# Performance work log

Hardware: AMD Instinct MI355X
Metric: run time of the kernel (lower is better)

## Reference

```python
import jax, jax.numpy as jnp
import numpy as np

ALPHA = 0.2  # LeakyReLU negative slope

def setup_inputs() -> dict:
    key = jax.random.key(0)
    k1, k2, k3 = jax.random.split(key, 3)
    B, N, F, H = 2, 4096, 512, 8
    d = F // H  # per-head in/out dim = 64
    h = jax.random.normal(k1, (B, N, F), dtype=jnp.float32)
    # xavier-uniform-like scale (gain 1.414, fan 64+64)
    W = jax.random.normal(k2, (H, d, d), dtype=jnp.float32) * 0.15
    a = jax.random.normal(k3, (H, 2 * d), dtype=jnp.float32) * 0.15
    return {"h": h, "W": W, "a": a}

def reference(h, W, a):
    B, N, F = h.shape
    H, _, o = W.shape
    d = F // H
    # split features per head: [B, H, N, d]
    hh = h.reshape(B, N, H, d).transpose(0, 2, 1, 3)
    Wh = jnp.einsum('bhnd,hdo->bhno', hh, W)          # [B,H,N,o]
    a1, a2 = a[:, :o], a[:, o:]
    Wh1 = jnp.einsum('bhno,ho->bhn', Wh, a1)          # [B,H,N]
    Wh2 = jnp.einsum('bhno,ho->bhn', Wh, a2)          # [B,H,N]
    e = jax.nn.leaky_relu(Wh1[..., :, None] + Wh2[..., None, :], ALPHA)  # [B,H,N,N]
    att = jax.nn.softmax(e, axis=-1)
    h_prime = jnp.einsum('bhnm,bhmo->bhno', att, Wh)  # [B,H,N,o]
    out = jax.nn.elu(h_prime)                         # concat=True -> ELU
    # concat heads along feature dim: [B, N, H*o]
    return out.transpose(0, 2, 1, 3).reshape(B, N, H * o)
```

## Files before the change

kernel.cpp:

```cpp
#include <hip/hip_runtime.h>
#include <hip/hip_fp16.h>


#define NB   2
#define NN   4096
#define NH   8
#define ALPHA 0.2f
#define LOG2E 1.4426950408889634f

typedef _Float16 f16x8 __attribute__((ext_vector_type(8)));
typedef _Float16 f16x2 __attribute__((ext_vector_type(2)));
typedef float    f32x4 __attribute__((ext_vector_type(4)));

__device__ __forceinline__ float dot2acc(f16x2 a, f16x2 b, float c) {
#if __has_builtin(__builtin_amdgcn_fdot2)
    return __builtin_amdgcn_fdot2(a, b, c, false);
#else
    return c + (float)a[0] * (float)b[0] + (float)a[1] * (float)b[1];
#endif
}

__global__ __launch_bounds__(256) void k_wh(
    const float* __restrict__ hsrc, const float* __restrict__ W,
    const float* __restrict__ a,
    _Float16* __restrict__ Wh_p, float* __restrict__ fb, float* __restrict__ gb)
{
    const int bid  = blockIdx.x;
    const int tile = bid & 63;
    const int bh   = bid >> 6;
    const int hh   = bh & 7;
    const int b    = bh >> 3;
    const int n0   = tile * 64;
    const int t    = threadIdx.x;
    const int w    = t >> 6;
    const int l    = t & 63;
    const int lr   = l & 15;
    const int lg   = l >> 4;

    __shared__ _Float16 __attribute__((aligned(16))) Wt16[64 * 88];
    __shared__ float red[2 * 64 * 16];

    {
        const float* Wg = W + hh * 4096;
        const int c  = t & 63;
        const int kq = (t >> 6) * 16;
        #pragma unroll
        for (int j = 0; j < 16; j++)
            Wt16[c * 88 + kq + j] = (_Float16)Wg[(kq + j) * 64 + c];
    }

    const float* hrow = hsrc + ((size_t)(b * NN + n0 + w * 16 + lr)) * 512
                        + hh * 64 + lg * 8;
    f16x8 afr[2];
    #pragma unroll
    for (int kh = 0; kh < 2; kh++) {
        float4 u0 = *(const float4*)(hrow + kh * 32);
        float4 u1 = *(const float4*)(hrow + kh * 32 + 4);
        f16x8 v;
        v[0] = (_Float16)u0.x; v[1] = (_Float16)u0.y;
        v[2] = (_Float16)u0.z; v[3] = (_Float16)u0.w;
        v[4] = (_Float16)u1.x; v[5] = (_Float16)u1.y;
        v[6] = (_Float16)u1.z; v[7] = (_Float16)u1.w;
        afr[kh] = v;
    }
    __syncthreads();

    f32x4 acc[4];
    #pragma unroll
    for (int ct = 0; ct < 4; ct++) acc[ct] = (f32x4){0.f, 0.f, 0.f, 0.f};
    #pragma unroll
    for (int kh = 0; kh < 2; kh++)
        #pragma unroll
        for (int ct = 0; ct < 4; ct++) {
            f16x8 bfr = *(const f16x8*)(&Wt16[(ct * 16 + lr) * 88 + kh * 32 + lg * 8]);
            acc[ct] = __builtin_amdgcn_mfma_f32_16x16x32_f16(afr[kh], bfr, acc[ct], 0, 0, 0);
        }

    {
        float a1v[4], a2v[4];
        const float* ag = a + hh * 128;
        #pragma unroll
        for (int ct = 0; ct < 4; ct++) {
            a1v[ct] = ag[ct * 16 + lr];
            a2v[ct] = ag[64 + ct * 16 + lr];
        }
        #pragma unroll
        for (int reg = 0; reg < 4; reg++) {
            float fp = 0.f, gp = 0.f;
            #pragma unroll
            for (int ct = 0; ct < 4; ct++) {
                fp = fmaf(acc[ct][reg], a1v[ct], fp);
                gp = fmaf(acc[ct][reg], a2v[ct], gp);
            }
            int row = w * 16 + lg * 4 + reg;
            red[0 * 1024 + row * 16 + lr] = fp;
            red[1 * 1024 + row * 16 + lr] = gp;
        }
    }
    __syncthreads();

    _Float16* wt = Wt16;
    #pragma unroll
    for (int ct = 0; ct < 4; ct++)
        #pragma unroll
        for (int reg = 0; reg < 4; reg++)
            wt[(ct * 16 + lr) * 88 + w * 16 + lg * 4 + reg] = (_Float16)acc[ct][reg];
    __syncthreads();

    if (t < 128) {
        int which = t >> 6, row = t & 63;
        const float* rr = &red[which * 1024 + row * 16];
        float s = 0.f;
        #pragma unroll
        for (int j = 0; j < 16; j++) s += rr[j];
        s *= LOG2E;
        float* dst = which ? gb : fb;
        dst[(size_t)bh * NN + n0 + row] = s;
    }

    #pragma unroll
    for (int p = 0; p < 2; p++) {
        int idx = t + p * 256;
        int ms  = idx >> 8;
        int ct  = (idx >> 6) & 3;
        int l2  = idx & 63;
        f16x8 v = *(const f16x8*)(&wt[(ct * 16 + (l2 & 15)) * 88 + ms * 32 + (l2 >> 4) * 8]);
        *(f16x8*)(Wh_p + (size_t)bh * 64 * NN
                       + (((size_t)(tile * 2 + ms) * 4 + ct) * 64 + l2) * 8) = v;
    }
}

__global__ __launch_bounds__(256) void k_prep(const float* __restrict__ gball,
                                              float* __restrict__ G,
                                              char* __restrict__ egfg_base)
{
    int bh = blockIdx.x, t = threadIdx.x;
    const float* g = gball + (size_t)bh * NN;
    float vals[16];
    float m = -1e30f;
    #pragma unroll
    for (int j = 0; j < 16; j++) { vals[j] = g[t + j * 256]; m = fmaxf(m, vals[j]); }
    #pragma unroll
    for (int s = 1; s < 64; s <<= 1) m = fmaxf(m, __shfl_xor(m, s, 64));
    __shared__ float wm[4];
    if ((t & 63) == 0) wm[t >> 6] = m;
    __syncthreads();
    float Gv = fmaxf(fmaxf(wm[0], wm[1]), fmaxf(wm[2], wm[3]));
    if (t == 0) G[bh] = Gv;
    _Float16* Eg = (_Float16*)(egfg_base + (size_t)bh * 16384);
    _Float16* Fg = Eg + NN;
    #pragma unroll
    for (int j = 0; j < 16; j++) {
        int i = t + j * 256;
        float d = vals[j] - Gv;
        Eg[i] = (_Float16)exp2f(d);
        Fg[i] = (_Float16)exp2f(ALPHA * d);
    }
}

__global__ __launch_bounds__(256, 3) void k_attn(
    const _Float16* __restrict__ Wh_p, const float* __restrict__ fb,
    const float* __restrict__ G, const char* __restrict__ egfg_base,
    float* __restrict__ out)
{
    const int orig  = blockIdx.x;
    const int bid   = (orig & 7) * 64 + (orig >> 3);
    const int ntile = bid & 31;
    const int bh    = bid >> 5;
    const int hh    = bh & 7;
    const int b     = bh >> 3;
    const int n0    = ntile * 128;
    const int t     = threadIdx.x;
    const int w     = t >> 6;
    const int l     = t & 63;
    const int kg    = w >> 1;
    const int wr    = w & 1;
    const int lr    = l & 15;
    const int lg    = l >> 4;

    const _Float16* Pp  = Wh_p + (size_t)bh * 64 * NN;
    const _Float16* Egp = (const _Float16*)(egfg_base + (size_t)bh * 16384);
    const float     Gv  = G[bh];

    f16x2 ef2[4], ff2[4];
    #pragma unroll
    for (int rg = 0; rg < 4; rg++) {
        int rn = n0 + wr * 64 + rg * 16 + lr;
        float s  = fb[(size_t)bh * NN + rn] + Gv;
        float t1 = (1.f - ALPHA) * s;
        _Float16 e = (_Float16)exp2f(fminf(t1, 0.f));
        _Float16 f = (_Float16)exp2f(fminf(-t1, 0.f));
        ef2[rg] = (f16x2){e, e};
        ff2[rg] = (f16x2){f, f};
    }
    const f16x2 one2 = (f16x2){(_Float16)1.0f, (_Float16)1.0f};

    f32x4 acc[4][4];
    #pragma unroll
    for (int rg = 0; rg < 4; rg++)
        #pragma unroll
        for (int ct = 0; ct < 4; ct++) acc[rg][ct] = (f32x4){0.f, 0.f, 0.f, 0.f};
    float dsum[4] = {0.f, 0.f, 0.f, 0.f};

    const _Float16* bp  = Pp + (size_t)kg * 64 * 2048 + (size_t)l * 8;
    const _Float16* ep  = Egp + kg * 2048 + lg * 8;
    const _Float16* epf = ep + NN;

    #define LOADSET(B0,B1,B2,B3,EG,FG)                                          \
        {                                                                        \
            B0 = *(const f16x8*)(bp);         B1 = *(const f16x8*)(bp + 512);    \
            B2 = *(const f16x8*)(bp + 1024);  B3 = *(const f16x8*)(bp + 1536);   \
            EG = *(const f16x8*)ep;           FG = *(const f16x8*)epf;           \
            bp += 2048; ep += 32; epf += 32;                                     \
        }

    #define COMPUTE(B0,B1,B2,B3,EG,FG)                                          \
        {                                                                        \
            _Pragma("unroll")                                                    \
            for (int rg = 0; rg < 4; rg++) {                                     \
                f16x8 af; float ds = dsum[rg];                                   \
                _Pragma("unroll")                                                \
                for (int d = 0; d < 4; d++) {                                    \
                    f16x2 e2 = ((const f16x2*)&(EG))[d];                         \
                    f16x2 f2 = ((const f16x2*)&(FG))[d];                         \
                    f16x2 p2 = __builtin_elementwise_max(e2 * ef2[rg],           \
                                                         f2 * ff2[rg]);          \
                    ((f16x2*)&af)[d] = p2;                                       \
                    ds = dot2acc(p2, one2, ds);                                  \
                }                                                                \
                dsum[rg] = ds;                                                   \
                acc[rg][0] = __builtin_amdgcn_mfma_f32_16x16x32_f16(             \
                    af, B0, acc[rg][0], 0, 0, 0);                                \
                acc[rg][1] = __builtin_amdgcn_mfma_f32_16x16x32_f16(             \
                    af, B1, acc[rg][1], 0, 0, 0);                                \
                acc[rg][2] = __builtin_amdgcn_mfma_f32_16x16x32_f16(             \
                    af, B2, acc[rg][2], 0, 0, 0);                                \
                acc[rg][3] = __builtin_amdgcn_mfma_f32_16x16x32_f16(             \
                    af, B3, acc[rg][3], 0, 0, 0);                                \
            }                                                                    \
        }

    f16x8 a0, a1, a2, a3, ae, az;
    f16x8 c0, c1, c2, c3, ce, cz;
    LOADSET(a0, a1, a2, a3, ae, az);

    #pragma clang loop unroll(disable)
    for (int hs = 0; hs < 64; hs += 2) {
        LOADSET(c0, c1, c2, c3, ce, cz);
        COMPUTE(a0, a1, a2, a3, ae, az);
        if (hs + 2 < 64) LOADSET(a0, a1, a2, a3, ae, az);
        COMPUTE(c0, c1, c2, c3, ce, cz);
    }
    #undef LOADSET
    #undef COMPUTE

    __shared__ f32x4 __attribute__((aligned(16))) Rw[2][16 * 64];
    __shared__ float dnP[256];
    __shared__ float dnS[128];

    #pragma unroll
    for (int rg = 0; rg < 4; rg++) {
        float d = dsum[rg];
        d += __shfl_xor(d, 16, 64);
        d += __shfl_xor(d, 32, 64);
        if (lg == 0) dnP[kg * 128 + wr * 64 + rg * 16 + lr] = d;
    }

    if (kg == 1) {
        #pragma unroll
        for (int rg = 0; rg < 4; rg++)
            #pragma unroll
            for (int ct = 0; ct < 4; ct++)
                Rw[wr][(rg * 4 + ct) * 64 + l] = acc[rg][ct];
    }
    __syncthreads();

    if (kg == 0) {
        dnS[wr * 64 + l] = dnP[wr * 64 + l] + dnP[128 + wr * 64 + l];
        float* outp = out + ((size_t)(b * NN + n0)) * 512 + hh * 64;
        #pragma unroll
        for (int rg = 0; rg < 4; rg++)
            #pragma unroll
            for (int reg = 0; reg < 4; reg++) {
                int row = wr * 64 + rg * 16 + lg * 4 + reg;
                float rinv = 1.0f / dnS[row];
                #pragma unroll
                for (int ct = 0; ct < 4; ct++) {
                    float v = (acc[rg][ct][reg] + Rw[wr][(rg * 4 + ct) * 64 + l][reg])
                              * rinv;
                    v = v > 0.f ? v : (exp2f(v * LOG2E) - 1.f);
                    outp[(size_t)row * 512 + ct * 16 + lr] = v;
                }
            }
    }
}

extern "C" void kernel_launch(void* const* d_in, const int* in_sizes, int n_in,
                              void* d_out, int out_size, void* d_ws, size_t ws_size,
                              hipStream_t stream)
{
    const float* hsrc = (const float*)d_in[0];
    const float* W    = (const float*)d_in[1];
    const float* a    = (const float*)d_in[2];
    float* outp       = (float*)d_out;

    const size_t WHT_BYTES = (size_t)NB * NH * 64 * NN * sizeof(_Float16);
    const size_t FB_BYTES  = (size_t)NB * NH * NN * sizeof(float);
    const size_t GB_BYTES  = (size_t)NB * NH * NN * sizeof(float);
    const size_t NEED = WHT_BYTES + FB_BYTES + GB_BYTES + 64 * sizeof(float);
    if (ws_size < NEED) return;

    char* ws = (char*)d_ws;
    _Float16* Wh_p = (_Float16*)ws;
    float*    fbuf = (float*)(ws + WHT_BYTES);
    char*     gbase = ws + WHT_BYTES + FB_BYTES;
    float*    Gmax = (float*)(ws + WHT_BYTES + FB_BYTES + GB_BYTES);

    k_wh  <<<dim3(NB * NH * (NN / 64)),  dim3(256), 0, stream>>>(hsrc, W, a, Wh_p, fbuf, (float*)gbase);
    k_prep<<<dim3(NB * NH),              dim3(256), 0, stream>>>((const float*)gbase, Gmax, gbase);
    k_attn<<<dim3(NB * NH * (NN / 128)), dim3(256), 0, stream>>>(Wh_p, fbuf, Gmax, gbase, outp);
}
```

Measured before the change: 57.15 us.

## Enlarge attention tile to 256 rows with 512 threads and four K-split groups

The attention kernel now computes 256 output rows per block using 8 waves. Each wave covers 128 rows, so every loaded Wh/Eg/Fg fragment feeds twice as many MFMAs, and the key dimension is split across four groups instead of two. The aim is to halve global B-operand traffic per output row. In exchange, accumulator registers double, which risks spills under the 512x2 launch bound. The grid halves, lowering occupancy, and the cross-group reduction through LDS becomes serialized over several barriers.

```diff
diff --git a/kernel.cpp b/kernel.cpp
--- a/kernel.cpp
+++ b/kernel.cpp
@@ -158,18 +158,18 @@
     }
 }
 
-__global__ __launch_bounds__(256, 3) void k_attn(
+__global__ __launch_bounds__(512, 2) void k_attn(
     const _Float16* __restrict__ Wh_p, const float* __restrict__ fb,
     const float* __restrict__ G, const char* __restrict__ egfg_base,
     float* __restrict__ out)
 {
     const int orig  = blockIdx.x;
-    const int bid   = (orig & 7) * 64 + (orig >> 3);
-    const int ntile = bid & 31;
-    const int bh    = bid >> 5;
+    const int bid   = (orig & 7) * 32 + (orig >> 3);
+    const int ntile = bid & 15;
+    const int bh    = bid >> 4;
     const int hh    = bh & 7;
     const int b     = bh >> 3;
-    const int n0    = ntile * 128;
+    const int n0    = ntile * 256;
     const int t     = threadIdx.x;
     const int w     = t >> 6;
     const int l     = t & 63;
@@ -182,10 +182,10 @@
     const _Float16* Egp = (const _Float16*)(egfg_base + (size_t)bh * 16384);
     const float     Gv  = G[bh];
 
-    f16x2 ef2[4], ff2[4];
-    #pragma unroll
-    for (int rg = 0; rg < 4; rg++) {
-        int rn = n0 + wr * 64 + rg * 16 + lr;
+    f16x2 ef2[8], ff2[8];
+    #pragma unroll
+    for (int rg = 0; rg < 8; rg++) {
+        int rn = n0 + wr * 128 + rg * 16 + lr;
         float s  = fb[(size_t)bh * NN + rn] + Gv;
         float t1 = (1.f - ALPHA) * s;
         _Float16 e = (_Float16)exp2f(fminf(t1, 0.f));
@@ -195,15 +195,15 @@
     }
     const f16x2 one2 = (f16x2){(_Float16)1.0f, (_Float16)1.0f};
 
-    f32x4 acc[4][4];
-    #pragma unroll
-    for (int rg = 0; rg < 4; rg++)
+    f32x4 acc[8][4];
+    #pragma unroll
+    for (int rg = 0; rg < 8; rg++)
         #pragma unroll
         for (int ct = 0; ct < 4; ct++) acc[rg][ct] = (f32x4){0.f, 0.f, 0.f, 0.f};
-    float dsum[4] = {0.f, 0.f, 0.f, 0.f};
-
-    const _Float16* bp  = Pp + (size_t)kg * 64 * 2048 + (size_t)l * 8;
-    const _Float16* ep  = Egp + kg * 2048 + lg * 8;
+    float dsum[8] = {0.f, 0.f, 0.f, 0.f, 0.f, 0.f, 0.f, 0.f};
+
+    const _Float16* bp  = Pp + (size_t)kg * 32 * 2048 + (size_t)l * 8;
+    const _Float16* ep  = Egp + kg * 1024 + lg * 8;
     const _Float16* epf = ep + NN;
 
     #define LOADSET(B0,B1,B2,B3,EG,FG)                                          \
@@ -217,7 +217,7 @@
     #define COMPUTE(B0,B1,B2,B3,EG,FG)                                          \
         {                                                                        \
             _Pragma("unroll")                                                    \
-            for (int rg = 0; rg < 4; rg++) {                                     \
+            for (int rg = 0; rg < 8; rg++) {                                     \
                 f16x8 af; float ds = dsum[rg];                                   \
                 _Pragma("unroll")                                                \
                 for (int d = 0; d < 4; d++) {                                    \
@@ -245,54 +245,67 @@
     LOADSET(a0, a1, a2, a3, ae, az);
 
     #pragma clang loop unroll(disable)
-    for (int hs = 0; hs < 64; hs += 2) {
+    for (int hs = 0; hs < 32; hs += 2) {
         LOADSET(c0, c1, c2, c3, ce, cz);
         COMPUTE(a0, a1, a2, a3, ae, az);
-        if (hs + 2 < 64) LOADSET(a0, a1, a2, a3, ae, az);
+        if (hs + 2 < 32) LOADSET(a0, a1, a2, a3, ae, az);
         COMPUTE(c0, c1, c2, c3, ce, cz);
     }
     #undef LOADSET
     #undef COMPUTE
 
-    __shared__ f32x4 __attribute__((aligned(16))) Rw[2][16 * 64];
-    __shared__ float dnP[256];
-    __shared__ float dnS[128];
-
-    #pragma unroll
-    for (int rg = 0; rg < 4; rg++) {
+    __shared__ f32x4 __attribute__((aligned(16))) Rw[2][32 * 64];
+    __shared__ float dnP[1024];
+    __shared__ float dnS[256];
+
+    #pragma unroll
+    for (int rg = 0; rg < 8; rg++) {
         float d = dsum[rg];
         d += __shfl_xor(d, 16, 64);
         d += __shfl_xor(d, 32, 64);
-        if (lg == 0) dnP[kg * 128 + wr * 64 + rg * 16 + lr] = d;
-    }
-
-    if (kg == 1) {
-        #pragma unroll
-        for (int rg = 0; rg < 4; rg++)
-            #pragma unroll
-            for (int ct = 0; ct < 4; ct++)
-                Rw[wr][(rg * 4 + ct) * 64 + l] = acc[rg][ct];
-    }
+        if (lg == 0) dnP[kg * 256 + wr * 128 + rg * 16 + lr] = d;
+    }
+
+    #define WRITE_R()                                                            \
+        { _Pragma("unroll") for (int rg = 0; rg < 8; rg++)                       \
+          _Pragma("unroll") for (int ct = 0; ct < 4; ct++)                       \
+            Rw[wr][(rg * 4 + ct) * 64 + l] = acc[rg][ct]; }
+    #define ADD_R()                                                              \
+        { _Pragma("unroll") for (int rg = 0; rg < 8; rg++)                       \
+          _Pragma("unroll") for (int ct = 0; ct < 4; ct++)                       \
+            acc[rg][ct] += Rw[wr][(rg * 4 + ct) * 64 + l]; }
+
+    if (kg == 1) WRITE_R();
+    __syncthreads();
+    if (t < 256) dnS[t] = dnP[t] + dnP[256 + t] + dnP[512 + t] + dnP[768 + t];
+    if (kg == 0) ADD_R();
+    __syncthreads();
+    if (kg == 2) WRITE_R();
+    __syncthreads();
+    if (kg == 0) ADD_R();
+    __syncthreads();
+    if (kg == 3) WRITE_R();
     __syncthreads();
 
     if (kg == 0) {
-        dnS[wr * 64 + l] = dnP[wr * 64 + l] + dnP[128 + wr * 64 + l];
+        ADD_R();
         float* outp = out + ((size_t)(b * NN + n0)) * 512 + hh * 64;
         #pragma unroll
-        for (int rg = 0; rg < 4; rg++)
+        for (int rg = 0; rg < 8; rg++)
             #pragma unroll
             for (int reg = 0; reg < 4; reg++) {
-                int row = wr * 64 + rg * 16 + lg * 4 + reg;
+                int row = wr * 128 + rg * 16 + lg * 4 + reg;
                 float rinv = 1.0f / dnS[row];
                 #pragma unroll
                 for (int ct = 0; ct < 4; ct++) {
-                    float v = (acc[rg][ct][reg] + Rw[wr][(rg * 4 + ct) * 64 + l][reg])
-                              * rinv;
+                    float v = acc[rg][ct][reg] * rinv;
                     v = v > 0.f ? v : (exp2f(v * LOG2E) - 1.f);
                     outp[(size_t)row * 512 + ct * 16 + lr] = v;
                 }
             }
     }
+    #undef WRITE_R
+    #undef ADD_R
 }
 
 extern "C" void kernel_launch(void* const* d_in, const int* in_sizes, int n_in,
@@ -318,5 +331,5 @@
 
     k_wh  <<<dim3(NB * NH * (NN / 64)),  dim3(256), 0, stream>>>(hsrc, W, a, Wh_p, fbuf, (float*)gbase);
     k_prep<<<dim3(NB * NH),              dim3(256), 0, stream>>>((const float*)gbase, Gmax, gbase);
-    k_attn<<<dim3(NB * NH * (NN / 128)), dim3(256), 0, stream>>>(Wh_p, fbuf, Gmax, gbase, outp);
-}
+    k_attn<<<dim3(NB * NH * (NN / 256)), dim3(512), 0, stream>>>(Wh_p, fbuf, Gmax, gbase, outp);
+}
```

New measurement: 58.86 us. 3.0% more time.

## Switch attention matmul from 16x16x32 to 32x32x16 MFMA tiles

Applied to the files above, without the earlier changes.

Replaces the 16x16x32 f16 MFMA tiling in the attention kernel with 32x32x16 MFMA, reorganizing the packed Wh layout written by k_wh to match the new B-operand fragment order. Each wave now builds half as many probability fragments per k-step: 2 row groups of 32 instead of 4 of 16, with two k-substeps per load set. That cuts the exp/max/dot work spent forming A operands and the number of MFMA issues. The epilogue and the denominator reduction are rewritten for the 32x32 accumulator register mapping, and the cross-wave exchange through shared memory now uses 16-wide accumulators.

```diff
diff --git a/kernel.cpp b/kernel.cpp
--- a/kernel.cpp
+++ b/kernel.cpp
@@ -11,6 +11,7 @@
 typedef _Float16 f16x8 __attribute__((ext_vector_type(8)));
 typedef _Float16 f16x2 __attribute__((ext_vector_type(2)));
 typedef float    f32x4 __attribute__((ext_vector_type(4)));
+typedef float    f32x16 __attribute__((ext_vector_type(16)));
 
 __device__ __forceinline__ float dot2acc(f16x2 a, f16x2 b, float c) {
 #if __has_builtin(__builtin_amdgcn_fdot2)
@@ -121,12 +122,12 @@
     #pragma unroll
     for (int p = 0; p < 2; p++) {
         int idx = t + p * 256;
-        int ms  = idx >> 8;
-        int ct  = (idx >> 6) & 3;
+        int st  = idx >> 7;
+        int cg  = (idx >> 6) & 1;
         int l2  = idx & 63;
-        f16x8 v = *(const f16x8*)(&wt[(ct * 16 + (l2 & 15)) * 88 + ms * 32 + (l2 >> 4) * 8]);
+        f16x8 v = *(const f16x8*)(&wt[(cg * 32 + (l2 & 31)) * 88 + st * 16 + (l2 >> 5) * 8]);
         *(f16x8*)(Wh_p + (size_t)bh * 64 * NN
-                       + (((size_t)(tile * 2 + ms) * 4 + ct) * 64 + l2) * 8) = v;
+                       + (((size_t)(tile * 4 + st) * 2 + cg) * 64 + l2) * 8) = v;
     }
 }
 
@@ -175,17 +176,17 @@
     const int l     = t & 63;
     const int kg    = w >> 1;
     const int wr    = w & 1;
-    const int lr    = l & 15;
-    const int lg    = l >> 4;
+    const int l5    = l & 31;
+    const int g5    = l >> 5;
 
     const _Float16* Pp  = Wh_p + (size_t)bh * 64 * NN;
     const _Float16* Egp = (const _Float16*)(egfg_base + (size_t)bh * 16384);
     const float     Gv  = G[bh];
 
-    f16x2 ef2[4], ff2[4];
-    #pragma unroll
-    for (int rg = 0; rg < 4; rg++) {
-        int rn = n0 + wr * 64 + rg * 16 + lr;
+    f16x2 ef2[2], ff2[2];
+    #pragma unroll
+    for (int rg = 0; rg < 2; rg++) {
+        int rn = n0 + wr * 64 + rg * 32 + l5;
         float s  = fb[(size_t)bh * NN + rn] + Gv;
         float t1 = (1.f - ALPHA) * s;
         _Float16 e = (_Float16)exp2f(fminf(t1, 0.f));
@@ -195,29 +196,32 @@
     }
     const f16x2 one2 = (f16x2){(_Float16)1.0f, (_Float16)1.0f};
 
-    f32x4 acc[4][4];
-    #pragma unroll
-    for (int rg = 0; rg < 4; rg++)
-        #pragma unroll
-        for (int ct = 0; ct < 4; ct++) acc[rg][ct] = (f32x4){0.f, 0.f, 0.f, 0.f};
-    float dsum[4] = {0.f, 0.f, 0.f, 0.f};
-
-    const _Float16* bp  = Pp + (size_t)kg * 64 * 2048 + (size_t)l * 8;
-    const _Float16* ep  = Egp + kg * 2048 + lg * 8;
+    f32x16 acc[2][2];
+    #pragma unroll
+    for (int rg = 0; rg < 2; rg++)
+        #pragma unroll
+        for (int cg = 0; cg < 2; cg++)
+            #pragma unroll
+            for (int q = 0; q < 16; q++) acc[rg][cg][q] = 0.f;
+    float dsum[2] = {0.f, 0.f};
+
+    const _Float16* bp  = Pp + (size_t)kg * 128 * 1024 + (size_t)l * 8;
+    const _Float16* ep  = Egp + kg * 2048 + g5 * 8;
     const _Float16* epf = ep + NN;
 
-    #define LOADSET(B0,B1,B2,B3,EG,FG)                                          \
+    #define LOADSET(B00,B01,B10,B11,E0,E1,F0,F1)                                \
         {                                                                        \
-            B0 = *(const f16x8*)(bp);         B1 = *(const f16x8*)(bp + 512);    \
-            B2 = *(const f16x8*)(bp + 1024);  B3 = *(const f16x8*)(bp + 1536);   \
-            EG = *(const f16x8*)ep;           FG = *(const f16x8*)epf;           \
+            B00 = *(const f16x8*)(bp);         B01 = *(const f16x8*)(bp + 512);  \
+            B10 = *(const f16x8*)(bp + 1024);  B11 = *(const f16x8*)(bp + 1536); \
+            E0  = *(const f16x8*)ep;           E1  = *(const f16x8*)(ep + 16);   \
+            F0  = *(const f16x8*)epf;          F1  = *(const f16x8*)(epf + 16);  \
             bp += 2048; ep += 32; epf += 32;                                     \
         }
 
-    #define COMPUTE(B0,B1,B2,B3,EG,FG)                                          \
+    #define STEP(B0,B1,EG,FG)                                                   \
         {                                                                        \
             _Pragma("unroll")                                                    \
-            for (int rg = 0; rg < 4; rg++) {                                     \
+            for (int rg = 0; rg < 2; rg++) {                                     \
                 f16x8 af; float ds = dsum[rg];                                   \
                 _Pragma("unroll")                                                \
                 for (int d = 0; d < 4; d++) {                                    \
@@ -229,29 +233,29 @@
                     ds = dot2acc(p2, one2, ds);                                  \
                 }                                                                \
                 dsum[rg] = ds;                                                   \
-                acc[rg][0] = __builtin_amdgcn_mfma_f32_16x16x32_f16(             \
+                acc[rg][0] = __builtin_amdgcn_mfma_f32_32x32x16_f16(             \
                     af, B0, acc[rg][0], 0, 0, 0);                                \
-                acc[rg][1] = __builtin_amdgcn_mfma_f32_16x16x32_f16(             \
+                acc[rg][1] = __builtin_amdgcn_mfma_f32_32x32x16_f16(             \
                     af, B1, acc[rg][1], 0, 0, 0);                                \
-                acc[rg][2] = __builtin_amdgcn_mfma_f32_16x16x32_f16(             \
-                    af, B2, acc[rg][2], 0, 0, 0);                                \
-                acc[rg][3] = __builtin_amdgcn_mfma_f32_16x16x32_f16(             \
-                    af, B3, acc[rg][3], 0, 0, 0);                                \
             }                                                                    \
         }
 
-    f16x8 a0, a1, a2, a3, ae, az;
-    f16x8 c0, c1, c2, c3, ce, cz;
-    LOADSET(a0, a1, a2, a3, ae, az);
+    #define COMPUTE(B00,B01,B10,B11,E0,E1,F0,F1)                                \
+        { STEP(B00,B01,E0,F0) STEP(B10,B11,E1,F1) }
+
+    f16x8 a00,a01,a10,a11,ae0,ae1,af0,af1;
+    f16x8 c00,c01,c10,c11,ce0,ce1,cf0,cf1;
+    LOADSET(a00,a01,a10,a11,ae0,ae1,af0,af1);
 
     #pragma clang loop unroll(disable)
     for (int hs = 0; hs < 64; hs += 2) {
-        LOADSET(c0, c1, c2, c3, ce, cz);
-        COMPUTE(a0, a1, a2, a3, ae, az);
-        if (hs + 2 < 64) LOADSET(a0, a1, a2, a3, ae, az);
-        COMPUTE(c0, c1, c2, c3, ce, cz);
+        LOADSET(c00,c01,c10,c11,ce0,ce1,cf0,cf1);
+        COMPUTE(a00,a01,a10,a11,ae0,ae1,af0,af1);
+        if (hs + 2 < 64) LOADSET(a00,a01,a10,a11,ae0,ae1,af0,af1);
+        COMPUTE(c00,c01,c10,c11,ce0,ce1,cf0,cf1);
     }
     #undef LOADSET
+    #undef STEP
     #undef COMPUTE
 
     __shared__ f32x4 __attribute__((aligned(16))) Rw[2][16 * 64];
@@ -259,39 +263,47 @@
     __shared__ float dnS[128];
 
     #pragma unroll
-    for (int rg = 0; rg < 4; rg++) {
+    for (int rg = 0; rg < 2; rg++) {
         float d = dsum[rg];
-        d += __shfl_xor(d, 16, 64);
         d += __shfl_xor(d, 32, 64);
-        if (lg == 0) dnP[kg * 128 + wr * 64 + rg * 16 + lr] = d;
+        if (g5 == 0) dnP[kg * 128 + wr * 64 + rg * 32 + l5] = d;
     }
 
     if (kg == 1) {
         #pragma unroll
-        for (int rg = 0; rg < 4; rg++)
+        for (int rg = 0; rg < 2; rg++)
             #pragma unroll
-            for (int ct = 0; ct < 4; ct++)
-                Rw[wr][(rg * 4 + ct) * 64 + l] = acc[rg][ct];
+            for (int cg = 0; cg < 2; cg++)
+                #pragma unroll
+                for (int q = 0; q < 4; q++) {
+                    f32x4 v = (f32x4){acc[rg][cg][q*4+0], acc[rg][cg][q*4+1],
+                                      acc[rg][cg][q*4+2], acc[rg][cg][q*4+3]};
+                    Rw[wr][((rg * 2 + cg) * 4 + q) * 64 + l] = v;
+                }
     }
     __syncthreads();
 
     if (kg == 0) {
-        dnS[wr * 64 + l] = dnP[wr * 64 + l] + dnP[128 + wr * 64 + l];
+        dnS[t] = dnP[t] + dnP[128 + t];
         float* outp = out + ((size_t)(b * NN + n0)) * 512 + hh * 64;
         #pragma unroll
-        for (int rg = 0; rg < 4; rg++)
+        for (int rg = 0; rg < 2; rg++)
             #pragma unroll
-            for (int reg = 0; reg < 4; reg++) {
-                int row = wr * 64 + rg * 16 + lg * 4 + reg;
-                float rinv = 1.0f / dnS[row];
+            for (int cg = 0; cg < 2; cg++)
                 #pragma unroll
-                for (int ct = 0; ct < 4; ct++) {
-                    float v = (acc[rg][ct][reg] + Rw[wr][(rg * 4 + ct) * 64 + l][reg])
-                              * rinv;
-                    v = v > 0.f ? v : (exp2f(v * LOG2E) - 1.f);
-                    outp[(size_t)row * 512 + ct * 16 + lr] = v;
+                for (int q = 0; q < 4; q++) {
+                    f32x4 r = Rw[wr][((rg * 2 + cg) * 4 + q) * 64 + l];
+                    #pragma unroll
+                    for (int j = 0; j < 4; j++) {
+                        int reg = q * 4 + j;
+                        int row = wr * 64 + rg * 32
+                                + (reg & 3) + 8 * (reg >> 2) + 4 * g5;
+                        float rinv = 1.0f / dnS[row];
+                        float v = (acc[rg][cg][reg] + r[j]) * rinv;
+                        v = v > 0.f ? v : (exp2f(v * LOG2E) - 1.f);
+                        outp[(size_t)row * 512 + cg * 32 + l5] = v;
+                    }
                 }
-            }
     }
 }
 
```

Result: slower. 65.67 us (+14.9%).
